# Optimization experiments

Measured on AMD Instinct MI355X. Metric: run time of the kernel, lower is better.

## Reference

```python
import jax, jax.numpy as jnp
import numpy as np

N = 25000      # nodes
E = 400000     # directed edges (avg degree 16)
F_IN = 133     # atom feature dim (QM_137k)
H = 8          # heads
C = 64         # hidden per head
HC = H * C     # 512
OUT = 1
NEG_SLOPE = 0.2
BN_EPS = 1e-5


def setup_inputs() -> dict:
    key = jax.random.key(0)
    ks = jax.random.split(key, 8)
    s = 0.05
    return {
        "x": jax.random.normal(ks[0], (N, F_IN), jnp.float32),
        "edge_index": jax.random.randint(ks[1], (2, E), 0, N, dtype=jnp.int32),
        # GATv2Conv params (share_weights=False): W_l for src, W_r for dst, att vector per head
        "Wl": jax.random.normal(ks[2], (F_IN, HC), jnp.float32) * s,
        "Wr": jax.random.normal(ks[3], (F_IN, HC), jnp.float32) * s,
        "att": jax.random.normal(ks[4], (H, C), jnp.float32) * s,
        "b1": jnp.zeros((HC,), jnp.float32),
        # BatchNorm1d (eval mode: running stats)
        "bn_gamma": jnp.ones((HC,), jnp.float32),
        "bn_beta": jnp.zeros((HC,), jnp.float32),
        "bn_mean": jnp.zeros((HC,), jnp.float32),
        "bn_var": jnp.ones((HC,), jnp.float32),
        # PReLU (default: single shared weight, init 0.25)
        "prelu_w": jnp.full((1,), 0.25, jnp.float32),
        # GCNConv params
        "Wg": jax.random.normal(ks[5], (HC, OUT), jnp.float32) * s,
        "bg": jnp.zeros((OUT,), jnp.float32),
    }


def _with_self_loops(edge_index):
    loops = jnp.arange(N, dtype=edge_index.dtype)
    src = jnp.concatenate([edge_index[0], loops])
    dst = jnp.concatenate([edge_index[1], loops])
    return src, dst


def _gatv2(x, edge_index, Wl, Wr, att, b1):
    # PyG GATv2Conv, concat=True, add_self_loops=True, eval (attention dropout off)
    src, dst = _with_self_loops(edge_index)
    xl = (x @ Wl).reshape(N, H, C)   # source-side transform
    xr = (x @ Wr).reshape(N, H, C)   # target-side transform
    msg = xl[src]                    # [E', H, C] gathered source messages
    e = jnp.einsum('ehc,hc->eh', jax.nn.leaky_relu(msg + xr[dst], NEG_SLOPE), att)  # [E', H]
    # segment softmax over incoming edges of each dst node (self loops => no empty segments)
    emax = jax.ops.segment_max(e, dst, num_segments=N)
    ee = jnp.exp(e - emax[dst])
    den = jax.ops.segment_sum(ee, dst, num_segments=N)
    agg = jax.ops.segment_sum(ee[:, :, None] * msg, dst, num_segments=N)  # [N, H, C]
    out = agg / den[:, :, None]
    return out.reshape(N, HC) + b1


def _gcn(x, edge_index, Wg, bg):
    # PyG GCNConv: add self loops, sym-normalized aggregation of x @ W, plus bias
    src, dst = _with_self_loops(edge_index)
    deg = jax.ops.segment_sum(jnp.ones_like(dst, dtype=x.dtype), dst, num_segments=N)
    dinv = jax.lax.rsqrt(jnp.maximum(deg, 1.0))
    h = x @ Wg                                   # [N, OUT]
    norm = dinv[src] * dinv[dst]                 # [E']
    return jax.ops.segment_sum(norm[:, None] * h[src], dst, num_segments=N) + bg


def reference(x, edge_index, Wl, Wr, att, b1, bn_gamma, bn_beta, bn_mean, bn_var,
              prelu_w, Wg, bg):
    h = _gatv2(x, edge_index, Wl, Wr, att, b1)
    # BatchNorm1d (eval) + PReLU
    h = (h - bn_mean) * jax.lax.rsqrt(bn_var + BN_EPS) * bn_gamma + bn_beta
    h = jnp.where(h >= 0, h, prelu_w * h)
    # dropout is identity in eval mode
    out = _gcn(h, edge_index, Wg, bg)
    return out.squeeze()  # [N]
```

## Files before the change

kernel.cpp:

```cpp
#include <hip/hip_runtime.h>

#define NN 25000
#define EE 400000
#define FIN 133
#define HCC 512
#define RPAD 25088
#define KPAD 160
#define NT 5
#define CAP 64
#define EPB 4082

typedef __attribute__((ext_vector_type(8))) __bf16 bf16x8;
typedef __attribute__((ext_vector_type(4))) float f32x4;
typedef __attribute__((ext_vector_type(8))) _Float16 f16x8;
typedef __attribute__((ext_vector_type(2))) _Float16 f16x2;

static __device__ __forceinline__ ushort f2bf(float f) {
    uint32_t u = __float_as_uint(f);
    uint32_t r = (u + 0x7fffu + ((u >> 16) & 1u)) >> 16;
    return (ushort)r;
}
static __device__ __forceinline__ float bf2f(ushort b) {
    return __uint_as_float(((uint32_t)b) << 16);
}

static __device__ __forceinline__ f16x2 lrelu2(f16x2 t) {
#if __has_builtin(__builtin_elementwise_max) && __has_builtin(__builtin_elementwise_min)
    const f16x2 z = {(_Float16)0.f, (_Float16)0.f};
    const f16x2 c = {(_Float16)0.2f, (_Float16)0.2f};
    return __builtin_elementwise_min(t, z) * c + __builtin_elementwise_max(t, z);
#else
    f16x2 r;
    r[0] = t[0] >= (_Float16)0.f ? t[0] : (_Float16)((float)t[0] * 0.2f);
    r[1] = t[1] >= (_Float16)0.f ? t[1] : (_Float16)((float)t[1] * 0.2f);
    return r;
#endif
}
static __device__ __forceinline__ float fdot2f(f16x2 a, f16x2 b, float c) {
#if __has_builtin(__builtin_amdgcn_fdot2)
    return __builtin_amdgcn_fdot2(a, b, c, false);
#else
    return c + (float)a[0] * (float)b[0] + (float)a[1] * (float)b[1];
#endif
}

__global__ __launch_bounds__(256) void k_prep(const float* __restrict__ x,
    const float* __restrict__ Wl, const float* __restrict__ Wr,
    ushort* __restrict__ ah, ushort* __restrict__ al,
    ushort* __restrict__ wh, ushort* __restrict__ wl)
{
    const int tid = threadIdx.x;
    const int y = blockIdx.y;
    if (y < 20) {
        const int row = blockIdx.x * 256 + tid;
        const int oct = y;
        const int kb = oct * 8;
        ushort h[8], l[8];
        #pragma unroll
        for (int j = 0; j < 8; ++j) {
            int k = kb + j;
            float v = (row < NN && k < FIN) ? x[(size_t)row * FIN + k] : 0.f;
            ushort hh = f2bf(v);
            h[j] = hh;
            l[j] = f2bf(v - bf2f(hh));
        }
        uint4 H, L;
        H.x = h[0] | (h[1] << 16); H.y = h[2] | (h[3] << 16);
        H.z = h[4] | (h[5] << 16); H.w = h[6] | (h[7] << 16);
        L.x = l[0] | (l[1] << 16); L.y = l[2] | (l[3] << 16);
        L.z = l[4] | (l[5] << 16); L.w = l[6] | (l[7] << 16);
        size_t slot = (size_t)oct * RPAD + row;
        ((uint4*)ah)[slot] = H;
        ((uint4*)al)[slot] = L;
    } else {
        if (blockIdx.x >= 80) return;
        const int oct = blockIdx.x >> 2;
        const int col = (blockIdx.x & 3) * 256 + tid;
        const int kb = oct * 8;
        const float* W = (col < 512) ? Wl : Wr;
        const int c = (col < 512) ? col : col - 512;
        ushort h[8], l[8];
        #pragma unroll
        for (int j = 0; j < 8; ++j) {
            int k = kb + j;
            float v = (k < FIN) ? W[(size_t)k * 512 + c] : 0.f;
            ushort hh = f2bf(v);
            h[j] = hh;
            l[j] = f2bf(v - bf2f(hh));
        }
        uint4 H, L;
        H.x = h[0] | (h[1] << 16); H.y = h[2] | (h[3] << 16);
        H.z = h[4] | (h[5] << 16); H.w = h[6] | (h[7] << 16);
        L.x = l[0] | (l[1] << 16); L.y = l[2] | (l[3] << 16);
        L.z = l[4] | (l[5] << 16); L.w = l[6] | (l[7] << 16);
        size_t slot = (size_t)oct * 1024 + col;
        ((uint4*)wh)[slot] = H;
        ((uint4*)wl)[slot] = L;
    }
}

__global__ __launch_bounds__(256, 2) void k_gemm3(
    const ushort* __restrict__ ah, const ushort* __restrict__ al,
    const ushort* __restrict__ wh, const ushort* __restrict__ wl,
    ushort* __restrict__ xl, float* __restrict__ xr,
    const int* __restrict__ srcp, const int* __restrict__ dstp,
    int* __restrict__ cnt, int* __restrict__ csr)
{
    if (blockIdx.y >= 196) {
        int sbid = (blockIdx.y - 196) * 8 + blockIdx.x;
        if (sbid < 98) {
            int e0 = sbid * EPB;
            int e1 = e0 + EPB; if (e1 > EE) e1 = EE;
            for (int e = e0 + threadIdx.x; e < e1; e += 256) {
                int d = dstp[e];
                int pos = atomicAdd(&cnt[d], 1);
                csr[d * CAP + pos] = srcp[e];
            }
        }
        return;
    }
    __shared__ __align__(16) ushort Ah[4096], Al[4096], Bh[4096], Bl[4096];
    const int tid = threadIdx.x;
    const int wid = tid >> 6, lane = tid & 63;
    const int row0 = blockIdx.y * 128;
    const int cb = blockIdx.x * 128;
    const bool isR = cb >= 512;
    const int oc0 = isR ? cb - 512 : cb;
    const int wr = wid >> 1, wc = wid & 1;
    const int s0 = tid, s1 = tid + 256;

    uint4 rah0, rah1, ral0, ral1, rbh0, rbh1, rbl0, rbl1;
    auto load = [&](int t) {
        int kg0 = s0 >> 7, i0 = s0 & 127;
        int kg1 = s1 >> 7, i1 = s1 & 127;
        size_t a0 = (size_t)(t * 4 + kg0) * RPAD + row0 + i0;
        size_t a1 = (size_t)(t * 4 + kg1) * RPAD + row0 + i1;
        size_t b0 = (size_t)(t * 4 + kg0) * 1024 + cb + i0;
        size_t b1 = (size_t)(t * 4 + kg1) * 1024 + cb + i1;
        rah0 = ((const uint4*)ah)[a0]; rah1 = ((const uint4*)ah)[a1];
        ral0 = ((const uint4*)al)[a0]; ral1 = ((const uint4*)al)[a1];
        rbh0 = ((const uint4*)wh)[b0]; rbh1 = ((const uint4*)wh)[b1];
        rbl0 = ((const uint4*)wl)[b0]; rbl1 = ((const uint4*)wl)[b1];
    };

    f32x4 acc[4][4];
    #pragma unroll
    for (int i = 0; i < 4; ++i)
        #pragma unroll
        for (int j = 0; j < 4; ++j) acc[i][j] = (f32x4)0.f;

    load(0);
    for (int t = 0; t < NT; ++t) {
        __syncthreads();
        ((uint4*)Ah)[s0] = rah0; ((uint4*)Ah)[s1] = rah1;
        ((uint4*)Al)[s0] = ral0; ((uint4*)Al)[s1] = ral1;
        ((uint4*)Bh)[s0] = rbh0; ((uint4*)Bh)[s1] = rbh1;
        ((uint4*)Bl)[s0] = rbl0; ((uint4*)Bl)[s1] = rbl1;
        __syncthreads();
        if (t + 1 < NT) load(t + 1);
        const int kg = lane >> 4, r = lane & 15;
        bf16x8 fah[4], fal[4], fbh[4], fbl[4];
        #pragma unroll
        for (int i = 0; i < 4; ++i) {
            int sa = kg * 128 + wr * 64 + i * 16 + r;
            fah[i] = *(const bf16x8*)&Ah[sa * 8];
            fal[i] = *(const bf16x8*)&Al[sa * 8];
            int sb = kg * 128 + wc * 64 + i * 16 + r;
            fbh[i] = *(const bf16x8*)&Bh[sb * 8];
            fbl[i] = *(const bf16x8*)&Bl[sb * 8];
        }
        #pragma unroll
        for (int i = 0; i < 4; ++i)
            #pragma unroll
            for (int j = 0; j < 4; ++j)
                acc[i][j] = __builtin_amdgcn_mfma_f32_16x16x32_bf16(fah[i], fbh[j], acc[i][j], 0, 0, 0);
        #pragma unroll
        for (int i = 0; i < 4; ++i)
            #pragma unroll
            for (int j = 0; j < 4; ++j)
                acc[i][j] = __builtin_amdgcn_mfma_f32_16x16x32_bf16(fah[i], fbl[j], acc[i][j], 0, 0, 0);
        #pragma unroll
        for (int i = 0; i < 4; ++i)
            #pragma unroll
            for (int j = 0; j < 4; ++j)
                acc[i][j] = __builtin_amdgcn_mfma_f32_16x16x32_bf16(fal[i], fbh[j], acc[i][j], 0, 0, 0);
    }
    const int cl = lane & 15, rq = lane >> 4;
    #pragma unroll
    for (int i = 0; i < 4; ++i) {
        #pragma unroll
        for (int rr = 0; rr < 4; ++rr) {
            int row = row0 + wr * 64 + i * 16 + rq * 4 + rr;
            if (row < NN) {
                if (isR) {
                    #pragma unroll
                    for (int j = 0; j < 4; ++j)
                        xr[(size_t)row * HCC + oc0 + wc * 64 + j * 16 + cl] = acc[i][j][rr];
                } else {
                    #pragma unroll
                    for (int j = 0; j < 4; ++j) {
                        _Float16 hv = (_Float16)acc[i][j][rr];
                        xl[(size_t)row * HCC + oc0 + wc * 64 + j * 16 + cl] =
                            *(const ushort*)&hv;
                    }
                }
            }
        }
    }
}

__global__ __launch_bounds__(256) void k_gat(
    const ushort* __restrict__ xl, const float* __restrict__ xr,
    const float* __restrict__ att, const float* __restrict__ b1,
    const float* __restrict__ gam, const float* __restrict__ bet,
    const float* __restrict__ mean, const float* __restrict__ var,
    const float* __restrict__ pw, const float* __restrict__ Wg,
    const int* __restrict__ cnt, const int* __restrict__ csr,
    float* __restrict__ g, float* __restrict__ dinvp)
{
    const int lane = threadIdx.x & 63;
    const int node = blockIdx.x * 4 + (threadIdx.x >> 6);
    const int sb = lane * 8;
    float4 x0 = *(const float4*)&xr[(size_t)node * HCC + sb];
    float4 x1 = *(const float4*)&xr[(size_t)node * HCC + sb + 4];
    float4 a0 = *(const float4*)&att[sb];
    float4 a1 = *(const float4*)&att[sb + 4];
    f16x2 xrh[4], avh[4];
    xrh[0] = {(_Float16)x0.x, (_Float16)x0.y};
    xrh[1] = {(_Float16)x0.z, (_Float16)x0.w};
    xrh[2] = {(_Float16)x1.x, (_Float16)x1.y};
    xrh[3] = {(_Float16)x1.z, (_Float16)x1.w};
    avh[0] = {(_Float16)a0.x, (_Float16)a0.y};
    avh[1] = {(_Float16)a0.z, (_Float16)a0.w};
    avh[2] = {(_Float16)a1.x, (_Float16)a1.y};
    avh[3] = {(_Float16)a1.z, (_Float16)a1.w};
    float s = 0.f;
    float acc[8] = {0.f, 0.f, 0.f, 0.f, 0.f, 0.f, 0.f, 0.f};
    const int deg = cnt[node];
    const int beg = node * CAP;
    auto process = [&](f16x8 hv) {
        const f16x2* hp = (const f16x2*)&hv;
        float ep = 0.f;
        #pragma unroll
        for (int p = 0; p < 4; ++p) {
            f16x2 t = hp[p] + xrh[p];
            ep = fdot2f(lrelu2(t), avh[p], ep);
        }
        ep += __shfl_xor(ep, 1);
        ep += __shfl_xor(ep, 2);
        ep += __shfl_xor(ep, 4);
        float w = __expf(ep);
        s += w;
        const _Float16* he = (const _Float16*)&hv;
        #pragma unroll
        for (int k = 0; k < 8; ++k) acc[k] += w * (float)he[k];
    };
    auto row = [&](int srcn) -> f16x8 {
        return *(const f16x8*)&xl[(size_t)srcn * HCC + sb];
    };
    process(row(node));
    int j = 0;
    for (; j + 4 <= deg; j += 4) {
        int sA = csr[beg + j], sB = csr[beg + j + 1];
        int sC = csr[beg + j + 2], sD = csr[beg + j + 3];
        f16x8 hA = row(sA);
        f16x8 hB = row(sB);
        f16x8 hC = row(sC);
        f16x8 hD = row(sD);
        process(hA); process(hB); process(hC); process(hD);
    }
    for (; j < deg; ++j) process(row(csr[beg + j]));
    float inv = 1.f / s;
    float p_w = pw[0];
    float dot = 0.f;
    #pragma unroll
    for (int k = 0; k < 8; ++k) {
        int idx = sb + k;
        float v = acc[k] * inv + b1[idx];
        v = (v - mean[idx]) * rsqrtf(var[idx] + 1e-5f) * gam[idx] + bet[idx];
        v = v >= 0.f ? v : p_w * v;
        dot += v * Wg[idx];
    }
    dot += __shfl_xor(dot, 1);
    dot += __shfl_xor(dot, 2);
    dot += __shfl_xor(dot, 4);
    dot += __shfl_xor(dot, 8);
    dot += __shfl_xor(dot, 16);
    dot += __shfl_xor(dot, 32);
    if (lane == 0) {
        float dn = rsqrtf((float)(deg + 1));
        g[node] = dn * dot;
        dinvp[node] = dn;
    }
}

__global__ __launch_bounds__(256) void k_gcn(
    const float* __restrict__ g, const float* __restrict__ dinv,
    const int* __restrict__ cnt, const int* __restrict__ csr,
    const float* __restrict__ bg, float* __restrict__ out)
{
    int t = blockIdx.x * 256 + threadIdx.x;
    int node = t >> 2;
    int sub = t & 3;
    if (node >= NN) return;
    int deg = cnt[node];
    int base = node * CAP;
    float s = 0.f;
    for (int j = sub; j < deg; j += 4) s += g[csr[base + j]];
    s += __shfl_xor(s, 1);
    s += __shfl_xor(s, 2);
    if (sub == 0) out[node] = dinv[node] * (g[node] + s) + bg[0];
}

extern "C" void kernel_launch(void* const* d_in, const int* in_sizes, int n_in,
                              void* d_out, int out_size, void* d_ws, size_t ws_size,
                              hipStream_t stream)
{
    const float* x    = (const float*)d_in[0];
    const int*   ei   = (const int*)d_in[1];
    const float* Wl   = (const float*)d_in[2];
    const float* Wr   = (const float*)d_in[3];
    const float* att  = (const float*)d_in[4];
    const float* b1   = (const float*)d_in[5];
    const float* gam  = (const float*)d_in[6];
    const float* bet  = (const float*)d_in[7];
    const float* mean = (const float*)d_in[8];
    const float* var  = (const float*)d_in[9];
    const float* pw   = (const float*)d_in[10];
    const float* Wg   = (const float*)d_in[11];
    const float* bg   = (const float*)d_in[12];
    float* out = (float*)d_out;

    char* base = (char*)d_ws;
    size_t o = 0;
    ushort* xl  = (ushort*)(base + o); o += (size_t)NN * HCC * 2;
    o = (o + 15) & ~(size_t)15;
    float* xr   = (float*)(base + o); o += (size_t)NN * HCC * 4;
    float* g    = (float*)(base + o); o += NN * 4;
    float* dinv = (float*)(base + o); o += NN * 4;
    int*   cnt  = (int*)(base + o);   o += NN * 4;
    int*   csr  = (int*)(base + o);   o += (size_t)NN * CAP * 4;
    o = (o + 15) & ~(size_t)15;
    ushort* ah = (ushort*)(base + o); o += (size_t)RPAD * KPAD * 2;
    ushort* al = (ushort*)(base + o); o += (size_t)RPAD * KPAD * 2;
    ushort* wh = (ushort*)(base + o); o += (size_t)KPAD * 1024 * 2;
    ushort* wl = (ushort*)(base + o); o += (size_t)KPAD * 1024 * 2;

    const int* srcp = ei;
    const int* dstp = ei + EE;

    hipMemsetAsync(cnt, 0, NN * sizeof(int), stream);
    k_prep<<<dim3(98, 21), 256, 0, stream>>>(x, Wl, Wr, ah, al, wh, wl);
    k_gemm3<<<dim3(8, 209), 256, 0, stream>>>(ah, al, wh, wl, xl, xr,
                                              srcp, dstp, cnt, csr);
    k_gat<<<NN / 4, 256, 0, stream>>>(xl, xr, att, b1, gam, bet, mean, var, pw, Wg,
                                      cnt, csr, g, dinv);
    k_gcn<<<(NN * 4 + 255) / 256, 256, 0, stream>>>(g, dinv, cnt, csr, bg, out);
}
```

Baseline: 226.8 us.

## Load GEMM fragments directly from global memory and store xr in fp16

```diff
diff --git a/kernel.cpp b/kernel.cpp
--- a/kernel.cpp
+++ b/kernel.cpp
@@ -99,10 +99,10 @@
     }
 }
 
-__global__ __launch_bounds__(256, 2) void k_gemm3(
+__global__ __launch_bounds__(256, 3) void k_gemm3(
     const ushort* __restrict__ ah, const ushort* __restrict__ al,
     const ushort* __restrict__ wh, const ushort* __restrict__ wl,
-    ushort* __restrict__ xl, float* __restrict__ xr,
+    ushort* __restrict__ xl, ushort* __restrict__ xr,
     const int* __restrict__ srcp, const int* __restrict__ dstp,
     int* __restrict__ cnt, int* __restrict__ csr)
 {
@@ -119,7 +119,6 @@
         }
         return;
     }
-    __shared__ __align__(16) ushort Ah[4096], Al[4096], Bh[4096], Bl[4096];
     const int tid = threadIdx.x;
     const int wid = tid >> 6, lane = tid & 63;
     const int row0 = blockIdx.y * 128;
@@ -127,21 +126,10 @@
     const bool isR = cb >= 512;
     const int oc0 = isR ? cb - 512 : cb;
     const int wr = wid >> 1, wc = wid & 1;
-    const int s0 = tid, s1 = tid + 256;
-
-    uint4 rah0, rah1, ral0, ral1, rbh0, rbh1, rbl0, rbl1;
-    auto load = [&](int t) {
-        int kg0 = s0 >> 7, i0 = s0 & 127;
-        int kg1 = s1 >> 7, i1 = s1 & 127;
-        size_t a0 = (size_t)(t * 4 + kg0) * RPAD + row0 + i0;
-        size_t a1 = (size_t)(t * 4 + kg1) * RPAD + row0 + i1;
-        size_t b0 = (size_t)(t * 4 + kg0) * 1024 + cb + i0;
-        size_t b1 = (size_t)(t * 4 + kg1) * 1024 + cb + i1;
-        rah0 = ((const uint4*)ah)[a0]; rah1 = ((const uint4*)ah)[a1];
-        ral0 = ((const uint4*)al)[a0]; ral1 = ((const uint4*)al)[a1];
-        rbh0 = ((const uint4*)wh)[b0]; rbh1 = ((const uint4*)wh)[b1];
-        rbl0 = ((const uint4*)wl)[b0]; rbl1 = ((const uint4*)wl)[b1];
-    };
+    const int kg = lane >> 4, r = lane & 15;
+
+    const int arow = row0 + wr * 64 + r;
+    const int bcol = cb + wc * 64 + r;
 
     f32x4 acc[4][4];
     #pragma unroll
@@ -149,25 +137,17 @@
         #pragma unroll
         for (int j = 0; j < 4; ++j) acc[i][j] = (f32x4)0.f;
 
-    load(0);
+    #pragma unroll
     for (int t = 0; t < NT; ++t) {
-        __syncthreads();
-        ((uint4*)Ah)[s0] = rah0; ((uint4*)Ah)[s1] = rah1;
-        ((uint4*)Al)[s0] = ral0; ((uint4*)Al)[s1] = ral1;
-        ((uint4*)Bh)[s0] = rbh0; ((uint4*)Bh)[s1] = rbh1;
-        ((uint4*)Bl)[s0] = rbl0; ((uint4*)Bl)[s1] = rbl1;
-        __syncthreads();
-        if (t + 1 < NT) load(t + 1);
-        const int kg = lane >> 4, r = lane & 15;
+        const size_t abase = (size_t)(t * 4 + kg) * RPAD + arow;
+        const size_t bbase = (size_t)(t * 4 + kg) * 1024 + bcol;
         bf16x8 fah[4], fal[4], fbh[4], fbl[4];
         #pragma unroll
         for (int i = 0; i < 4; ++i) {
-            int sa = kg * 128 + wr * 64 + i * 16 + r;
-            fah[i] = *(const bf16x8*)&Ah[sa * 8];
-            fal[i] = *(const bf16x8*)&Al[sa * 8];
-            int sb = kg * 128 + wc * 64 + i * 16 + r;
-            fbh[i] = *(const bf16x8*)&Bh[sb * 8];
-            fbl[i] = *(const bf16x8*)&Bl[sb * 8];
+            fah[i] = ((const bf16x8*)ah)[abase + i * 16];
+            fal[i] = ((const bf16x8*)al)[abase + i * 16];
+            fbh[i] = ((const bf16x8*)wh)[bbase + i * 16];
+            fbl[i] = ((const bf16x8*)wl)[bbase + i * 16];
         }
         #pragma unroll
         for (int i = 0; i < 4; ++i)
@@ -185,6 +165,7 @@
             for (int j = 0; j < 4; ++j)
                 acc[i][j] = __builtin_amdgcn_mfma_f32_16x16x32_bf16(fal[i], fbh[j], acc[i][j], 0, 0, 0);
     }
+    ushort* __restrict__ outp = isR ? xr : xl;
     const int cl = lane & 15, rq = lane >> 4;
     #pragma unroll
     for (int i = 0; i < 4; ++i) {
@@ -192,17 +173,11 @@
         for (int rr = 0; rr < 4; ++rr) {
             int row = row0 + wr * 64 + i * 16 + rq * 4 + rr;
             if (row < NN) {
-                if (isR) {
-                    #pragma unroll
-                    for (int j = 0; j < 4; ++j)
-                        xr[(size_t)row * HCC + oc0 + wc * 64 + j * 16 + cl] = acc[i][j][rr];
-                } else {
-                    #pragma unroll
-                    for (int j = 0; j < 4; ++j) {
-                        _Float16 hv = (_Float16)acc[i][j][rr];
-                        xl[(size_t)row * HCC + oc0 + wc * 64 + j * 16 + cl] =
-                            *(const ushort*)&hv;
-                    }
+                #pragma unroll
+                for (int j = 0; j < 4; ++j) {
+                    _Float16 hv = (_Float16)acc[i][j][rr];
+                    outp[(size_t)row * HCC + oc0 + wc * 64 + j * 16 + cl] =
+                        *(const ushort*)&hv;
                 }
             }
         }
@@ -210,7 +185,7 @@
 }
 
 __global__ __launch_bounds__(256) void k_gat(
-    const ushort* __restrict__ xl, const float* __restrict__ xr,
+    const ushort* __restrict__ xl, const ushort* __restrict__ xr,
     const float* __restrict__ att, const float* __restrict__ b1,
     const float* __restrict__ gam, const float* __restrict__ bet,
     const float* __restrict__ mean, const float* __restrict__ var,
@@ -221,15 +196,14 @@
     const int lane = threadIdx.x & 63;
     const int node = blockIdx.x * 4 + (threadIdx.x >> 6);
     const int sb = lane * 8;
-    float4 x0 = *(const float4*)&xr[(size_t)node * HCC + sb];
-    float4 x1 = *(const float4*)&xr[(size_t)node * HCC + sb + 4];
+    f16x8 xv = *(const f16x8*)&xr[(size_t)node * HCC + sb];
     float4 a0 = *(const float4*)&att[sb];
     float4 a1 = *(const float4*)&att[sb + 4];
     f16x2 xrh[4], avh[4];
-    xrh[0] = {(_Float16)x0.x, (_Float16)x0.y};
-    xrh[1] = {(_Float16)x0.z, (_Float16)x0.w};
-    xrh[2] = {(_Float16)x1.x, (_Float16)x1.y};
-    xrh[3] = {(_Float16)x1.z, (_Float16)x1.w};
+    {
+        const f16x2* xp = (const f16x2*)&xv;
+        xrh[0] = xp[0]; xrh[1] = xp[1]; xrh[2] = xp[2]; xrh[3] = xp[3];
+    }
     avh[0] = {(_Float16)a0.x, (_Float16)a0.y};
     avh[1] = {(_Float16)a0.z, (_Float16)a0.w};
     avh[2] = {(_Float16)a1.x, (_Float16)a1.y};
@@ -334,8 +308,8 @@
     char* base = (char*)d_ws;
     size_t o = 0;
     ushort* xl  = (ushort*)(base + o); o += (size_t)NN * HCC * 2;
+    ushort* xr  = (ushort*)(base + o); o += (size_t)NN * HCC * 2;
     o = (o + 15) & ~(size_t)15;
-    float* xr   = (float*)(base + o); o += (size_t)NN * HCC * 4;
     float* g    = (float*)(base + o); o += NN * 4;
     float* dinv = (float*)(base + o); o += NN * 4;
     int*   cnt  = (int*)(base + o);   o += NN * 4;
```

Result: faster. 220.8 us (-2.6%).
